# Performance work log

Hardware: AMD Instinct MI355X
Metric: run time of the kernel (lower is better)

## Reference

```python
import jax, jax.numpy as jnp
import numpy as np

EPS = 1e-8  # torch F.cosine_similarity eps


def _normalize(x):
    # x: [N, D]; clamp norm at eps like torch cosine_similarity
    n = jnp.linalg.norm(x, axis=-1, keepdims=True)
    return x / jnp.maximum(n, EPS)


def setup_inputs() -> dict:
    key = jax.random.key(0)
    k1, k2 = jax.random.split(key)
    N, D = 8192, 256
    return {
        "model_output": jax.random.normal(k1, (N, D), dtype=jnp.float32),
        "targets": jax.random.normal(k2, (N, D), dtype=jnp.float32),
        "weight": 1.0,
    }


def reference(model_output, targets, weight):
    # Pairwise cosine similarity via normalize + matmul (same math as
    # broadcasted cosine_similarity, without the O(N^2*D) intermediate).
    o = _normalize(model_output)          # [N, D]
    t = _normalize(targets)               # [N, D]
    sim_o = o @ o.T                       # [N, N]
    sim_t = t @ t.T                       # [N, N]
    n = sim_o.shape[0]
    mask = jnp.eye(n, dtype=bool)
    sim_o = jnp.where(mask, 0.0, sim_o)
    sim_t = jnp.where(mask, 0.0, sim_t)
    loss = jnp.mean((sim_o - sim_t) ** 2)
    return weight * loss
```

## Files before the change

### kernel.cpp

```cpp
#include <hip/hip_runtime.h>
#include <hip/hip_bf16.h>
#include <math.h>


#define N_ROWS 8192
#define DDIM   256
#define NC     32
#define KC     (N_ROWS / NC)
#define KS     64
#define NITER  (KC / KS)
#define PART_STRIDE 196608
#define NRED   192

#define OBT_UOFF  32
#define MAT_USZ   (DDIM * N_ROWS)
#define PART_UOFF (OBT_UOFF + 2 * MAT_USZ)

typedef __bf16 bf16x8 __attribute__((ext_vector_type(8)));
typedef short  short8 __attribute__((ext_vector_type(8)));
typedef unsigned short ushort8 __attribute__((ext_vector_type(8)));
typedef float  f32x16 __attribute__((ext_vector_type(16)));
typedef unsigned int u32;

__device__ inline unsigned short f2bu(float x) {
    __hip_bfloat16 h = __float2bfloat16(x);
    return __builtin_bit_cast(unsigned short, h);
}
__device__ inline float u2f(unsigned short u) {
    unsigned int v = ((unsigned int)u) << 16;
    return __builtin_bit_cast(float, v);
}
__device__ inline void gload_lds16(const void* g, void* l) {
    __builtin_amdgcn_global_load_lds(
        (const __attribute__((address_space(1))) u32*)g,
        (__attribute__((address_space(3))) u32*)l, 16, 0, 0);
}

__global__ __launch_bounds__(256) void transpose_kernel(const float* __restrict__ O,
                                                        const float* __restrict__ T,
                                                        float* __restrict__ ws) {
    int tid = threadIdx.x;
    if (blockIdx.x == 0 && tid == 0) {
        ws[0] = 0.0f;
        ((u32*)(ws + 4))[0] = 0u;
    }
    int b = blockIdx.x;
    const float* src = (b & 1) ? T : O;
    unsigned short* dst =
        (unsigned short*)ws + OBT_UOFF + (size_t)(b & 1) * MAT_USZ;
    int kb = (b >> 1) * 64;

    __shared__ unsigned short lt[64 * 256];
    int w = tid >> 6, l = tid & 63;
    #pragma unroll
    for (int j = 0; j < 16; ++j) {
        int r = j * 4 + w;
        float4 v = *reinterpret_cast<const float4*>(
            src + (size_t)(kb + r) * DDIM + l * 4);
        float ss = v.x * v.x + v.y * v.y + v.z * v.z + v.w * v.w;
        #pragma unroll
        for (int off = 32; off > 0; off >>= 1) ss += __shfl_xor(ss, off);
        float inv = 1.0f / fmaxf(sqrtf(ss), 1e-8f);
        ushort4 u;
        u.x = f2bu(v.x * inv); u.y = f2bu(v.y * inv);
        u.z = f2bu(v.z * inv); u.w = f2bu(v.w * inv);
        int idx = r * 256 + ((((l >> 1) ^ (r & 31)) << 3) | ((l & 1) << 2));
        *reinterpret_cast<ushort4*>(&lt[idx]) = u;
    }
    __syncthreads();
    #pragma unroll
    for (int s = 0; s < 8; ++s) {
        int f = (tid >> 3) + 32 * s;
        int kc = tid & 7;
        ushort8 u;
        #pragma unroll
        for (int j = 0; j < 8; ++j) {
            int k = kc * 8 + j;
            u[j] = lt[k * 256 + ((((f >> 3) ^ (k & 31)) << 3) | (f & 7))];
        }
        *reinterpret_cast<ushort8*>(&dst[(size_t)f * N_ROWS + kb + kc * 8]) = u;
    }
}

__global__ __launch_bounds__(256) void gram_kernel(float* __restrict__ ws) {
    const unsigned short* obt = (const unsigned short*)ws + OBT_UOFF;
    unsigned short* part = (unsigned short*)ws + PART_UOFF;

    int bid = blockIdx.x;
    int c  = (bid & 7) * 4 + (bid >> 7);
    int ti = (bid >> 3) & 15;
    int tm = ti >> 2, tn = ti & 3;
    int tid = threadIdx.x, lane = tid & 63, wid = tid >> 6;
    int wm = wid >> 1, wn = wid & 1;
    int k0 = c * KC;

    __shared__ __align__(16) unsigned short slabs[2][4][64 * KS];

    f32x16 acc_oo, acc_tt, acc_ot;
    #pragma unroll
    for (int e = 0; e < 16; ++e) { acc_oo[e] = 0.f; acc_tt[e] = 0.f; acc_ot[e] = 0.f; }

    int sl = wid;
    int mat = sl >> 1;
    int ft = (sl & 1) ? tn : tm;
    int frow = lane >> 3;
    int swz8 = ((lane & 7) ^ (frow & 7)) * 8;
    const unsigned short* slab_src =
        obt + (size_t)mat * MAT_USZ + (size_t)(ft * 64 + frow) * N_ROWS + swz8;

    auto stage = [&](int buf, int it) {
        int kb = k0 + it * KS;
        unsigned short* ld = &slabs[buf][sl][0];
        #pragma unroll
        for (int i = 0; i < 8; ++i)
            gload_lds16(slab_src + kb + (size_t)(i * 8) * N_ROWS, ld + i * 512);
    };

    int fm = wm * 32 + (lane & 31);
    int fn = wn * 32 + (lane & 31);
    int jhalf = lane >> 5;
    auto frag = [&](int buf, int s, int fl, int kk) -> bf16x8 {
        int j0 = kk * 2 + jhalf;
        const unsigned short* p = &slabs[buf][s][fl * KS + ((j0 ^ (fl & 7)) * 8)];
        return __builtin_bit_cast(bf16x8, *reinterpret_cast<const short8*>(p));
    };

    stage(0, 0);
    __syncthreads();
    int cur = 0;
    for (int it = 0; it < NITER; ++it) {
        if (it + 1 < NITER) stage(cur ^ 1, it + 1);
        #pragma unroll
        for (int kk = 0; kk < 4; ++kk) {
            bf16x8 ao = frag(cur, 0, fm, kk);
            bf16x8 bo = frag(cur, 1, fn, kk);
            bf16x8 at = frag(cur, 2, fm, kk);
            bf16x8 bt = frag(cur, 3, fn, kk);
            acc_oo = __builtin_amdgcn_mfma_f32_32x32x16_bf16(ao, bo, acc_oo, 0, 0, 0);
            acc_tt = __builtin_amdgcn_mfma_f32_32x32x16_bf16(at, bt, acc_tt, 0, 0, 0);
            acc_ot = __builtin_amdgcn_mfma_f32_32x32x16_bf16(ao, bt, acc_ot, 0, 0, 0);
        }
        __syncthreads();
        cur ^= 1;
    }

    unsigned int tb = (unsigned int)(c * 16 + ti) * 3;
    #pragma unroll
    for (int reg = 0; reg < 16; ++reg) {
        int row = (reg & 3) + 8 * (reg >> 2) + ((lane >> 5) << 2);
        int col = lane & 31;
        int idx = (wm * 32 + row) * 64 + (wn * 32 + col);
        part[(size_t)(tb + 0) * 4096 + idx] = f2bu(acc_oo[reg]);
        part[(size_t)(tb + 1) * 4096 + idx] = f2bu(acc_tt[reg]);
        part[(size_t)(tb + 2) * 4096 + idx] = f2bu(acc_ot[reg]);
    }
}

__global__ __launch_bounds__(256) void reduce_kernel(const float* __restrict__ W,
                                                     float* __restrict__ out,
                                                     float* __restrict__ ws) {
    const unsigned short* part = (const unsigned short*)ws + PART_UOFF;
    u32* ctr = (u32*)(ws + 4);
    int tid = threadIdx.x;
    int gid = blockIdx.x * 256 + tid;
    int base = gid * 4;
    float s0 = 0.f, s1 = 0.f, s2 = 0.f, s3 = 0.f;
    for (int cc = 0; cc < NC; ++cc) {
        ushort4 u = *reinterpret_cast<const ushort4*>(
            &part[(size_t)cc * PART_STRIDE + base]);
        s0 += u2f(u.x); s1 += u2f(u.y); s2 += u2f(u.z); s3 += u2f(u.w);
    }
    int g = (base >> 12) % 3;
    float s = s0 * s0 + s1 * s1 + s2 * s2 + s3 * s3;
    if (g == 2) s = -2.0f * s;
    #pragma unroll
    for (int off = 32; off > 0; off >>= 1) s += __shfl_down(s, off);
    __shared__ float wsum[4];
    int l = tid & 63, w = tid >> 6;
    if (l == 0) wsum[w] = s;
    __syncthreads();
    if (tid == 0) {
        atomicAdd(&ws[0], wsum[0] + wsum[1] + wsum[2] + wsum[3]);
        __threadfence();
        unsigned int r = atomicAdd(&ctr[0], 1u);
        if (r == NRED - 1) {
            float v = __hip_atomic_load(&ws[0], __ATOMIC_ACQUIRE,
                                        __HIP_MEMORY_SCOPE_AGENT);
            out[0] = v * W[0] / ((float)N_ROWS * (float)N_ROWS);
        }
    }
}

extern "C" void kernel_launch(void* const* d_in, const int* in_sizes, int n_in,
                              void* d_out, int out_size, void* d_ws, size_t ws_size,
                              hipStream_t stream) {
    const float* O = (const float*)d_in[0];
    const float* T = (const float*)d_in[1];
    const float* W = (const float*)d_in[2];
    float* out = (float*)d_out;
    float* ws = (float*)d_ws;

    transpose_kernel<<<256, 256, 0, stream>>>(O, T, ws);
    gram_kernel<<<512, 256, 0, stream>>>(ws);
    reduce_kernel<<<NRED, 256, 0, stream>>>(W, out, ws);
}
```

Baseline: 33.12 us.

## Use single-wave gram blocks loading MFMA fragments directly from global memory

The gram kernel moves from 256-thread blocks that stage 64-wide slabs through LDS with global_load_lds and barriers to 64-thread single-wave blocks. Each wave computes one 32x32 tile and reads its bf16 fragments straight from global memory, double-buffered in registers. The aim is to remove LDS staging and barrier overhead and to launch more, smaller blocks, at the cost of losing data reuse across waves and relying on L2 for repeated fragment reads. The transpose kernel swaps its XOR-swizzled LDS layout for padded rows with wider vector reads, and the reduce kernel uses 8-wide loads with half as many blocks.

```diff
diff --git a/kernel.cpp b/kernel.cpp
--- a/kernel.cpp
+++ b/kernel.cpp
@@ -7,10 +7,9 @@
 #define DDIM   256
 #define NC     32
 #define KC     (N_ROWS / NC)
-#define KS     64
-#define NITER  (KC / KS)
-#define PART_STRIDE 196608
-#define NRED   192
+#define NPOS   64
+#define PART_STRIDE (3 * NPOS * 1024)
+#define NRED   96
 
 #define OBT_UOFF  32
 #define MAT_USZ   (DDIM * N_ROWS)
@@ -18,7 +17,8 @@
 
 typedef __bf16 bf16x8 __attribute__((ext_vector_type(8)));
 typedef short  short8 __attribute__((ext_vector_type(8)));
-typedef unsigned short ushort8 __attribute__((ext_vector_type(8)));
+typedef unsigned short us4 __attribute__((ext_vector_type(4)));
+typedef unsigned short us8 __attribute__((ext_vector_type(8)));
 typedef float  f32x16 __attribute__((ext_vector_type(16)));
 typedef unsigned int u32;
 
@@ -29,11 +29,6 @@
 __device__ inline float u2f(unsigned short u) {
     unsigned int v = ((unsigned int)u) << 16;
     return __builtin_bit_cast(float, v);
-}
-__device__ inline void gload_lds16(const void* g, void* l) {
-    __builtin_amdgcn_global_load_lds(
-        (const __attribute__((address_space(1))) u32*)g,
-        (__attribute__((address_space(3))) u32*)l, 16, 0, 0);
 }
 
 __global__ __launch_bounds__(256) void transpose_kernel(const float* __restrict__ O,
@@ -50,7 +45,7 @@
         (unsigned short*)ws + OBT_UOFF + (size_t)(b & 1) * MAT_USZ;
     int kb = (b >> 1) * 64;
 
-    __shared__ unsigned short lt[64 * 256];
+    __shared__ unsigned short lt[64 * 260];
     int w = tid >> 6, l = tid & 63;
     #pragma unroll
     for (int j = 0; j < 16; ++j) {
@@ -61,98 +56,84 @@
         #pragma unroll
         for (int off = 32; off > 0; off >>= 1) ss += __shfl_xor(ss, off);
         float inv = 1.0f / fmaxf(sqrtf(ss), 1e-8f);
-        ushort4 u;
-        u.x = f2bu(v.x * inv); u.y = f2bu(v.y * inv);
-        u.z = f2bu(v.z * inv); u.w = f2bu(v.w * inv);
-        int idx = r * 256 + ((((l >> 1) ^ (r & 31)) << 3) | ((l & 1) << 2));
-        *reinterpret_cast<ushort4*>(&lt[idx]) = u;
+        us4 u;
+        u[0] = f2bu(v.x * inv); u[1] = f2bu(v.y * inv);
+        u[2] = f2bu(v.z * inv); u[3] = f2bu(v.w * inv);
+        *reinterpret_cast<us4*>(&lt[r * 260 + l * 4]) = u;
     }
     __syncthreads();
+    int ko = tid & 7;
+    int fq0 = tid >> 3;
     #pragma unroll
-    for (int s = 0; s < 8; ++s) {
-        int f = (tid >> 3) + 32 * s;
-        int kc = tid & 7;
-        ushort8 u;
+    for (int s = 0; s < 2; ++s) {
+        int fq = fq0 + 32 * s;
+        us4 rr[8];
         #pragma unroll
-        for (int j = 0; j < 8; ++j) {
-            int k = kc * 8 + j;
-            u[j] = lt[k * 256 + ((((f >> 3) ^ (k & 31)) << 3) | (f & 7))];
+        for (int j = 0; j < 8; ++j)
+            rr[j] = *reinterpret_cast<const us4*>(&lt[(ko * 8 + j) * 260 + fq * 4]);
+        #pragma unroll
+        for (int i = 0; i < 4; ++i) {
+            us8 o;
+            #pragma unroll
+            for (int j = 0; j < 8; ++j) o[j] = rr[j][i];
+            *reinterpret_cast<us8*>(
+                &dst[(size_t)(fq * 4 + i) * N_ROWS + kb + ko * 8]) = o;
         }
-        *reinterpret_cast<ushort8*>(&dst[(size_t)f * N_ROWS + kb + kc * 8]) = u;
     }
 }
 
-__global__ __launch_bounds__(256) void gram_kernel(float* __restrict__ ws) {
+__global__ __launch_bounds__(64) void gram_kernel(float* __restrict__ ws) {
     const unsigned short* obt = (const unsigned short*)ws + OBT_UOFF;
     unsigned short* part = (unsigned short*)ws + PART_UOFF;
 
     int bid = blockIdx.x;
-    int c  = (bid & 7) * 4 + (bid >> 7);
-    int ti = (bid >> 3) & 15;
-    int tm = ti >> 2, tn = ti & 3;
-    int tid = threadIdx.x, lane = tid & 63, wid = tid >> 6;
-    int wm = wid >> 1, wn = wid & 1;
-    int k0 = c * KC;
+    int c   = (bid & 7) * 4 + (bid >> 9);
+    int pos = (bid >> 3) & 63;
+    int pm = pos >> 3, pn = pos & 7;
+    int l = threadIdx.x;
 
-    __shared__ __align__(16) unsigned short slabs[2][4][64 * KS];
+    size_t fa = (size_t)(pm * 32 + (l & 31)) * N_ROWS;
+    size_t fb = (size_t)(pn * 32 + (l & 31)) * N_ROWS;
+    const unsigned short* Ao = obt + fa;
+    const unsigned short* Bo = obt + fb;
+    const unsigned short* At = obt + MAT_USZ + fa;
+    const unsigned short* Bt = obt + MAT_USZ + fb;
+    int kp = c * KC + ((l >> 5) * 8);
 
-    f32x16 acc_oo, acc_tt, acc_ot;
+    f32x16 aoo, att, aot;
     #pragma unroll
-    for (int e = 0; e < 16; ++e) { acc_oo[e] = 0.f; acc_tt[e] = 0.f; acc_ot[e] = 0.f; }
+    for (int e = 0; e < 16; ++e) { aoo[e] = 0.f; att[e] = 0.f; aot[e] = 0.f; }
 
-    int sl = wid;
-    int mat = sl >> 1;
-    int ft = (sl & 1) ? tn : tm;
-    int frow = lane >> 3;
-    int swz8 = ((lane & 7) ^ (frow & 7)) * 8;
-    const unsigned short* slab_src =
-        obt + (size_t)mat * MAT_USZ + (size_t)(ft * 64 + frow) * N_ROWS + swz8;
+#define BCK(p) __builtin_bit_cast(bf16x8, *reinterpret_cast<const short8*>(p))
+#define LDQ(A_, B_, C_, D_, s_) { int k = kp + (s_) * 16; \
+    A_ = BCK(Ao + k); B_ = BCK(Bo + k); C_ = BCK(At + k); D_ = BCK(Bt + k); }
+#define MMQ(A_, B_, C_, D_) { \
+    aoo = __builtin_amdgcn_mfma_f32_32x32x16_bf16(A_, B_, aoo, 0, 0, 0); \
+    att = __builtin_amdgcn_mfma_f32_32x32x16_bf16(C_, D_, att, 0, 0, 0); \
+    aot = __builtin_amdgcn_mfma_f32_32x32x16_bf16(A_, D_, aot, 0, 0, 0); }
 
-    auto stage = [&](int buf, int it) {
-        int kb = k0 + it * KS;
-        unsigned short* ld = &slabs[buf][sl][0];
-        #pragma unroll
-        for (int i = 0; i < 8; ++i)
-            gload_lds16(slab_src + kb + (size_t)(i * 8) * N_ROWS, ld + i * 512);
-    };
+    bf16x8 a0, b0, c0, d0, a1, b1, c1, d1;
+    LDQ(a0, b0, c0, d0, 0);
+    LDQ(a1, b1, c1, d1, 1);
+    #pragma unroll
+    for (int s = 0; s < 16; s += 2) {
+        MMQ(a0, b0, c0, d0);
+        if (s + 2 < 16) LDQ(a0, b0, c0, d0, s + 2);
+        MMQ(a1, b1, c1, d1);
+        if (s + 3 < 16) LDQ(a1, b1, c1, d1, s + 3);
+    }
+#undef BCK
+#undef LDQ
+#undef MMQ
 
-    int fm = wm * 32 + (lane & 31);
-    int fn = wn * 32 + (lane & 31);
-    int jhalf = lane >> 5;
-    auto frag = [&](int buf, int s, int fl, int kk) -> bf16x8 {
-        int j0 = kk * 2 + jhalf;
-        const unsigned short* p = &slabs[buf][s][fl * KS + ((j0 ^ (fl & 7)) * 8)];
-        return __builtin_bit_cast(bf16x8, *reinterpret_cast<const short8*>(p));
-    };
-
-    stage(0, 0);
-    __syncthreads();
-    int cur = 0;
-    for (int it = 0; it < NITER; ++it) {
-        if (it + 1 < NITER) stage(cur ^ 1, it + 1);
-        #pragma unroll
-        for (int kk = 0; kk < 4; ++kk) {
-            bf16x8 ao = frag(cur, 0, fm, kk);
-            bf16x8 bo = frag(cur, 1, fn, kk);
-            bf16x8 at = frag(cur, 2, fm, kk);
-            bf16x8 bt = frag(cur, 3, fn, kk);
-            acc_oo = __builtin_amdgcn_mfma_f32_32x32x16_bf16(ao, bo, acc_oo, 0, 0, 0);
-            acc_tt = __builtin_amdgcn_mfma_f32_32x32x16_bf16(at, bt, acc_tt, 0, 0, 0);
-            acc_ot = __builtin_amdgcn_mfma_f32_32x32x16_bf16(ao, bt, acc_ot, 0, 0, 0);
-        }
-        __syncthreads();
-        cur ^= 1;
-    }
-
-    unsigned int tb = (unsigned int)(c * 16 + ti) * 3;
+    size_t pb = (size_t)c * PART_STRIDE + (size_t)pos * 1024;
     #pragma unroll
     for (int reg = 0; reg < 16; ++reg) {
-        int row = (reg & 3) + 8 * (reg >> 2) + ((lane >> 5) << 2);
-        int col = lane & 31;
-        int idx = (wm * 32 + row) * 64 + (wn * 32 + col);
-        part[(size_t)(tb + 0) * 4096 + idx] = f2bu(acc_oo[reg]);
-        part[(size_t)(tb + 1) * 4096 + idx] = f2bu(acc_tt[reg]);
-        part[(size_t)(tb + 2) * 4096 + idx] = f2bu(acc_ot[reg]);
+        int row = (reg & 3) + 8 * (reg >> 2) + ((l >> 5) << 2);
+        int e = row * 32 + (l & 31);
+        part[pb + 0 * NPOS * 1024 + e] = f2bu(aoo[reg]);
+        part[pb + 1 * NPOS * 1024 + e] = f2bu(att[reg]);
+        part[pb + 2 * NPOS * 1024 + e] = f2bu(aot[reg]);
     }
 }
 
@@ -163,15 +144,19 @@
     u32* ctr = (u32*)(ws + 4);
     int tid = threadIdx.x;
     int gid = blockIdx.x * 256 + tid;
-    int base = gid * 4;
-    float s0 = 0.f, s1 = 0.f, s2 = 0.f, s3 = 0.f;
+    size_t base = (size_t)gid * 8;
+    float a[8];
+    #pragma unroll
+    for (int i = 0; i < 8; ++i) a[i] = 0.f;
     for (int cc = 0; cc < NC; ++cc) {
-        ushort4 u = *reinterpret_cast<const ushort4*>(
-            &part[(size_t)cc * PART_STRIDE + base]);
-        s0 += u2f(u.x); s1 += u2f(u.y); s2 += u2f(u.z); s3 += u2f(u.w);
+        us8 u = *reinterpret_cast<const us8*>(&part[(size_t)cc * PART_STRIDE + base]);
+        #pragma unroll
+        for (int i = 0; i < 8; ++i) a[i] += u2f(u[i]);
     }
-    int g = (base >> 12) % 3;
-    float s = s0 * s0 + s1 * s1 + s2 * s2 + s3 * s3;
+    float s = 0.f;
+    #pragma unroll
+    for (int i = 0; i < 8; ++i) s += a[i] * a[i];
+    int g = (int)(base >> 16);
     if (g == 2) s = -2.0f * s;
     #pragma unroll
     for (int off = 32; off > 0; off >>= 1) s += __shfl_down(s, off);
@@ -201,6 +186,6 @@
     float* ws = (float*)d_ws;
 
     transpose_kernel<<<256, 256, 0, stream>>>(O, T, ws);
-    gram_kernel<<<512, 256, 0, stream>>>(ws);
+    gram_kernel<<<2048, 64, 0, stream>>>(ws);
     reduce_kernel<<<NRED, 256, 0, stream>>>(W, out, ws);
 }
```

Measured after the change: 40.03 us. 20.9% more time.
